# Optimization experiments

Measured on AMD Instinct MI355X. Metric: run time of the kernel, lower is better.

The kernel has to match this reference:

```python
import jax, jax.numpy as jnp
import numpy as np

B, C_IN, H, W = 4, 256, 56, 56
REL, OUT, SP, K, PAD = 16, 256, 8, 7, 3
WS = OUT // SP            # 32 attention-weight channels
K2 = K * K                # 49 window taps
EPS = 1e-5


def _unfold(x, k, pad):
    # reflect-pad (SAN pad_mode=1 -> *_refpad kernels) then gather kxk window taps
    # x: [B,C,H,W] -> [B,C,k*k,H,W], tap order row-major (matches torch Unfold)
    xp = jnp.pad(x, ((0, 0), (0, 0), (pad, pad), (pad, pad)), mode='reflect')
    h, w = x.shape[2], x.shape[3]
    return jnp.stack([xp[:, :, i:i + h, j:j + w]
                      for i in range(k) for j in range(k)], axis=2)


def _conv1x1(x, w, b):
    return jnp.einsum('bchw,oc->bohw', x, w) + b[None, :, None, None]


def _bn(x, g, b, m, v):
    # eval-mode BatchNorm2d over channel axis 1, broadcast over trailing dims
    shape = (1, -1) + (1,) * (x.ndim - 2)
    scale = g.reshape(shape) * jax.lax.rsqrt(v.reshape(shape) + EPS)
    return (x - m.reshape(shape)) * scale + b.reshape(shape)


def _forward(x, w1, b1, w2, b2, w3, b3,
             bn1_g, bn1_b, bn1_m, bn1_v, cw1_w,
             bn2_g, bn2_b, bn2_m, bn2_v, cw2_w, cw2_b, pos2_w):
    x1 = _conv1x1(x, w1, b1)          # [B,REL,H,W]  (query)
    x2 = _conv1x1(x, w2, b2)          # [B,REL,H,W]  (key)
    x3 = _conv1x1(x, w3, b3)          # [B,OUT,H,W]  (value)

    # Subtraction2: q_i - k_j for each of K2 window taps -> [B,REL,K2,H,W]
    diff = x1[:, :, None, :, :] - _unfold(x2, K, PAAD) if False else x1[:, :, None, :, :] - _unfold(x2, K, PAD)

    # conv_w: BN -> ReLU -> 1x1 (no bias) -> BN -> ReLU -> 1x1 (bias)
    h = jax.nn.relu(_bn(diff, bn1_g, bn1_b, bn1_m, bn1_v))
    h = jnp.einsum('bckhw,oc->bokhw', h, cw1_w)
    h = jax.nn.relu(_bn(h, bn2_g, bn2_b, bn2_m, bn2_v))
    h = jnp.einsum('bckhw,oc->bokhw', h, cw2_w) + cw2_b[None, :, None, None, None]
    w = jax.nn.softmax(h, axis=2)     # softmax over K2 taps -> [B,WS,K2,H,W]

    # Aggregation: out[b,c,p] = sum_k unfold(x3)[b,c,k,p] * w[b, c//SP, k, p]
    unf3 = _unfold(x3, K, PAD).reshape(B, WS, SP, K2, H, W)
    agg = jnp.einsum('bgskhw,bgkhw->bgshw', unf3, w).reshape(B, OUT, H, W)

    # use_position2: interleave aggregated values with w, grouped 1x1 conv
    xv = agg.reshape(B, SP, WS, H, W).transpose(0, 2, 1, 3, 4)   # [B,WS,SP,H,W]
    xc = jnp.concatenate([xv, w], axis=2)                        # [B,WS,SP+K2,H,W]
    out = jnp.einsum('bgihw,goi->bgohw', xc, pos2_w).reshape(B, OUT, H, W)
    return out


def setup_inputs() -> dict:
    key = jax.random.key(0)
    ks = jax.random.split(key, 20)
    n = lambda k, s, sc=1.0: jax.random.normal(k, s, dtype=jnp.float32) * sc
    u = lambda k, s: jax.random.uniform(k, s, dtype=jnp.float32, minval=0.5, maxval=1.5)
    return {
        'x': n(ks[0], (B, C_IN, H, W)),
        'w1': n(ks[1], (REL, C_IN), 0.05), 'b1': n(ks[2], (REL,), 0.05),
        'w2': n(ks[3], (REL, C_IN), 0.05), 'b2': n(ks[4], (REL,), 0.05),
        'w3': n(ks[5], (OUT, C_IN), 0.05), 'b3': n(ks[6], (OUT,), 0.05),
        'bn1_g': u(ks[7], (REL,)), 'bn1_b': n(ks[8], (REL,), 0.1),
        'bn1_m': n(ks[9], (REL,), 0.1), 'bn1_v': u(ks[10], (REL,)),
        'cw1_w': n(ks[11], (REL, REL), 0.2),
        'bn2_g': u(ks[12], (REL,)), 'bn2_b': n(ks[13], (REL,), 0.1),
        'bn2_m': n(ks[14], (REL,), 0.1), 'bn2_v': u(ks[15], (REL,)),
        'cw2_w': n(ks[16], (WS, REL), 0.2), 'cw2_b': n(ks[17], (WS,), 0.05),
        'pos2_w': n(ks[18], (WS, SP, SP + K2), 0.1),
    }


def reference(x, w1, b1, w2, b2, w3, b3,
              bn1_g, bn1_b, bn1_m, bn1_v, cw1_w,
              bn2_g, bn2_b, bn2_m, bn2_v, cw2_w, cw2_b, pos2_w):
    return _forward(x, w1, b1, w2, b2, w3, b3,
                    bn1_g, bn1_b, bn1_m, bn1_v, cw1_w,
                    bn2_g, bn2_b, bn2_m, bn2_v, cw2_w, cw2_b, pos2_w)
```

## Files before the change

### kernel.cpp

```cpp
#include <hip/hip_runtime.h>

#define HW 56
#define NPIX 3136
#define CIN 256
#define OUTC 256

typedef unsigned short ushort_t;
typedef unsigned int uint_t;
typedef __attribute__((ext_vector_type(8))) short bf16x8;
typedef __attribute__((ext_vector_type(4))) float f32x4;
typedef __attribute__((ext_vector_type(2))) __fp16 half2v;

__device__ __forceinline__ ushort_t f2b(float f){
  uint_t u = __float_as_uint(f);
  u += 0x7fffu + ((u>>16)&1u);
  return (ushort_t)(u>>16);
}
__device__ __forceinline__ int refl(int v){ v = v<0 ? -v : v; return v>=HW ? 2*HW-2-v : v; }

#define BF_OFF   40960
#define CW1H_OFF 41280
#define CW2H_OFF 41536
#define CW2B_OFF 42048
#define BNC_OFF  42112
#define P2T_OFF  42176
#define P2H_OFF  56768
#define X1T_OFF  82368
#define X2T_OFF  283072
#define X3_BYTE_OFF 1935104

__global__ void k0_prep(const float* __restrict__ w1, const float* __restrict__ b1,
                        const float* __restrict__ w2, const float* __restrict__ b2,
                        const float* __restrict__ w3, const float* __restrict__ b3,
                        const float* __restrict__ g1, const float* __restrict__ be1,
                        const float* __restrict__ m1, const float* __restrict__ v1,
                        const float* __restrict__ cw1,
                        const float* __restrict__ g2, const float* __restrict__ be2,
                        const float* __restrict__ m2, const float* __restrict__ v2,
                        const float* __restrict__ cw2, const float* __restrict__ cw2b,
                        const float* __restrict__ p2,
                        float* __restrict__ ws)
{
  int idx = blockIdx.x*256 + threadIdx.x;
  if (idx < 81920){
    int j = idx & 7, l = (idx>>3)&63, t2 = idx>>9;
    int nf = t2 % 20, kt = t2 / 20;
    int k = kt*32 + (l>>4)*8 + j;
    int n = nf*16 + (l&15);
    float v = 0.f;
    if (n < 16)       v = w1[n*256 + k];
    else if (n < 32)  v = w2[(n-16)*256 + k];
    else if (n < 288) v = w3[(n-32)*256 + k];
    ((ushort_t*)ws)[idx] = f2b(v);
    return;
  }
  int j = idx - 81920;
  if (j < 288){ ws[BF_OFF+j] = (j<16 ? b1[j] : (j<32 ? b2[j-16] : b3[j-32])); return; }
  j -= 288;
  if (j < 32){ ws[BF_OFF+288+j] = 0.f; return; }
  j -= 32;
  if (j < 128){
    int o = j>>3, p = j&7;
    union { __fp16 h[2]; uint_t u; } cv;
    cv.h[0] = (__fp16)cw1[o*16 + 2*p];
    cv.h[1] = (__fp16)cw1[o*16 + 2*p+1];
    ((uint_t*)ws)[CW1H_OFF + j] = cv.u;
    return;
  }
  j -= 128;
  if (j < 256){
    int g = j>>3, p = j&7;
    union { __fp16 h[2]; uint_t u; } cv;
    cv.h[0] = (__fp16)cw2[g*16 + 2*p];
    cv.h[1] = (__fp16)cw2[g*16 + 2*p+1];
    ((uint_t*)ws)[CW2H_OFF + j] = cv.u;
    return;
  }
  j -= 256;
  if (j < 32){ ws[CW2B_OFF+j] = cw2b[j]; return; }
  j -= 32;
  if (j < 64){
    int set = j >> 4, c = j & 15;
    float o;
    if (set == 0){ o = g1[c] * rsqrtf(v1[c] + 1e-5f); }
    else if (set == 1){ float s = g1[c] * rsqrtf(v1[c] + 1e-5f); o = be1[c] - m1[c]*s; }
    else if (set == 2){ o = g2[c] * rsqrtf(v2[c] + 1e-5f); }
    else { float s = g2[c] * rsqrtf(v2[c] + 1e-5f); o = be2[c] - m2[c]*s; }
    ws[BNC_OFF+j] = o;
    return;
  }
  j -= 64;
  if (j < 14592){
    int i = j >> 8, rem = j & 255;
    ws[P2T_OFF + j] = p2[rem*57 + i];
    return;
  }
  j -= 14592;
  if (j < 25600){
    int p = j >> 8, c = j & 255;
    union { __fp16 h[2]; uint_t u; } cv;
    cv.h[0] = (__fp16)p2[c*57 + 8 + 2*p];
    cv.h[1] = (2*p+1 < 49) ? (__fp16)p2[c*57 + 9 + 2*p] : (__fp16)0.f;
    ((uint_t*)ws)[P2H_OFF + j] = cv.u;
    return;
  }
}

__global__ __launch_bounds__(256,2) void k1_proj(const float* __restrict__ x,
                                                 float* __restrict__ ws,
                                                 _Float16* __restrict__ x3h)
{
  __shared__ float xs[CIN*64];
  int t = threadIdx.x;
  int bid = blockIdx.x;
  int b = bid / 49, pp = (bid - b*49)*64;
  int wv = __builtin_amdgcn_readfirstlane(t >> 6);
  int lane = t & 63;

  {
    const float* src = x + (size_t)b*CIN*NPIX + pp;
    int c0 = t >> 4;
    int po = (t & 15) * 4;
    #pragma unroll
    for (int i=0;i<16;i++){
      const float* gp = src + (size_t)(i*16 + c0)*NPIX + po;
      __builtin_amdgcn_global_load_lds(
          (const __attribute__((address_space(1))) void*)gp,
          (__attribute__((address_space(3))) void*)(xs + i*1024 + wv*256),
          16, 0, 0);
    }
  }
  __syncthreads();

  f32x4 acc[4][5];
  float bias[5];
  #pragma unroll
  for (int nf=0;nf<5;nf++) bias[nf] = ws[BF_OFF + wv*80 + nf*16 + (lane&15)];
  #pragma unroll
  for (int m=0;m<4;m++)
    #pragma unroll
    for (int nf=0;nf<5;nf++)
      acc[m][nf] = (f32x4){bias[nf],bias[nf],bias[nf],bias[nf]};

  const uint4* bpk = (const uint4*)ws;
  #pragma unroll 1
  for (int kt=0;kt<8;kt++){
    int abase = (kt*32 + ((lane>>4)<<3))*64 + (lane&15);
    union { uint_t u[4]; bf16x8 v; } ahi[4], alo[4];
    #pragma unroll
    for (int m=0;m<4;m++){
      float f[8];
      #pragma unroll
      for (int j=0;j<8;j++) f[j] = xs[abase + j*64 + m*16];
      #pragma unroll
      for (int p=0;p<4;p++){
        uint_t u0 = __float_as_uint(f[2*p]), u1 = __float_as_uint(f[2*p+1]);
        uint_t h1 = u1 & 0xffff0000u;
        ahi[m].u[p] = (u0>>16) | h1;
        float l0 = f[2*p]   - __uint_as_float(u0 & 0xffff0000u);
        float l1 = f[2*p+1] - __uint_as_float(h1);
        alo[m].u[p] = (__float_as_uint(l0)>>16) | (__float_as_uint(l1) & 0xffff0000u);
      }
    }
    #pragma unroll
    for (int nf=0;nf<5;nf++){
      union { uint4 q; bf16x8 v; } bw;
      bw.q = bpk[(size_t)(kt*20 + wv*5 + nf)*64 + lane];
      #pragma unroll
      for (int m=0;m<4;m++){
        acc[m][nf] = __builtin_amdgcn_mfma_f32_16x16x32_bf16(ahi[m].v, bw.v, acc[m][nf], 0,0,0);
        acc[m][nf] = __builtin_amdgcn_mfma_f32_16x16x32_bf16(alo[m].v, bw.v, acc[m][nf], 0,0,0);
      }
    }
  }

  #pragma unroll
  for (int m=0;m<4;m++){
    #pragma unroll
    for (int r=0;r<4;r++){
      int sp = pp + m*16 + ((lane>>4)<<2) + r;
      #pragma unroll
      for (int nf=0;nf<5;nf++){
        int n = wv*80 + nf*16 + (lane&15);
        float val = acc[m][nf][r];
        if (n < 16){
          ws[X1T_OFF + (size_t)(b*NPIX + sp)*16 + n] = val;
        } else if (n < 32){
          ws[X2T_OFF + (size_t)(b*NPIX + sp)*16 + (n-16)] = val;
        } else if (n < 288){
          x3h[((size_t)b*NPIX + sp)*256 + (n-32)] = (_Float16)val;
        }
      }
    }
  }
}

__global__ __launch_bounds__(256,8) void k2_fused(const float* __restrict__ ws,
                                                  const _Float16* __restrict__ x3h,
                                                  float* __restrict__ out)
{
  __shared__ uint_t lgw[4*840];
  __shared__ int    gp_s[4*64];
  __shared__ __align__(16) float ags[4*256];

  int tid = threadIdx.x;
  int bid0 = blockIdx.x;
  int bid = (bid0 & 7)*392 + (bid0 >> 3);
  int b = bid / 784; int rem = bid - b*784;
  int row = rem / 14, xs4 = rem - row*14;
  int wv = __builtin_amdgcn_readfirstlane(tid >> 6);
  int lane = tid & 63;
  int y = row, x = xs4*4 + wv;
  int pix = y*HW + x;

  const float* bnc  = ws + BNC_OFF;
  const uint_t* c1h = (const uint_t*)ws + CW1H_OFF;
  const uint_t* c2h = (const uint_t*)ws + CW2H_OFF;
  const float* cw2b = ws + CW2B_OFF;
  uint_t* wvbase = lgw + wv*840;

  {
    int k = lane;
    int kk = k < 49 ? k : 48;
    int ki = kk / 7, kj = kk - ki*7;
    int gy = refl(y + ki - 3), gx = refl(x + kj - 3);
    int go = gy*HW + gx;
    gp_s[wv*64 + lane] = go;

    const float*  x1p = ws + X1T_OFF + (size_t)(b*NPIX + pix)*16;
    const float4* x2p = (const float4*)(ws + X2T_OFF + (size_t)(b*NPIX + go)*16);
    float4 v0 = x2p[0], v1 = x2p[1], v2 = x2p[2], v3 = x2p[3];
    float x2v[16] = {v0.x,v0.y,v0.z,v0.w, v1.x,v1.y,v1.z,v1.w,
                     v2.x,v2.y,v2.z,v2.w, v3.x,v3.y,v3.z,v3.w};
    float h1[16];
    #pragma unroll
    for (int c=0;c<16;c++){
      float d = x1p[c] - x2v[c];
      h1[c] = fmaxf(d*bnc[c] + bnc[16+c], 0.f);
    }
    half2v hp[8];
    #pragma unroll
    for (int p=0;p<8;p++) hp[p] = __builtin_amdgcn_cvt_pkrtz(h1[2*p], h1[2*p+1]);

    float tt[16];
    #pragma unroll
    for (int o=0;o<16;o++){
      float a = 0.f;
      #pragma unroll
      for (int p=0;p<8;p++){
        union { uint_t u; half2v h; } cv; cv.u = c1h[o*8+p];
        a = __builtin_amdgcn_fdot2(hp[p], cv.h, a, false);
      }
      tt[o] = fmaxf(a*bnc[32+o] + bnc[48+o], 0.f);
    }
    half2v tp[8];
    #pragma unroll
    for (int p=0;p<8;p++) tp[p] = __builtin_amdgcn_cvt_pkrtz(tt[2*p], tt[2*p+1]);

    if (k < 49){
      #pragma unroll
      for (int gp=0; gp<16; gp++){
        float a0 = cw2b[2*gp], a1 = cw2b[2*gp+1];
        #pragma unroll
        for (int p=0;p<8;p++){
          union { uint_t u; half2v h; } e0, e1;
          e0.u = c2h[(2*gp)*8+p];
          e1.u = c2h[(2*gp+1)*8+p];
          a0 = __builtin_amdgcn_fdot2(tp[p], e0.h, a0, false);
          a1 = __builtin_amdgcn_fdot2(tp[p], e1.h, a1, false);
        }
        union { half2v h; uint_t u; } pk;
        pk.h = __builtin_amdgcn_cvt_pkrtz(a0, a1);
        wvbase[k*17 + gp] = pk.u;
      }
    }
  }

  {
    int half = lane >> 5, g = lane & 31, gsel = g & 1, gp = g >> 1;
    float e[25];
    float M = -3.0e38f;
    #pragma unroll
    for (int i=0;i<25;i++){
      if (half == 0 || i < 24){
        uint_t u = wvbase[(half*25+i)*17 + gp];
        union { ushort_t s; __fp16 h; } cv;
        cv.s = gsel ? (ushort_t)(u>>16) : (ushort_t)(u & 0xffffu);
        e[i] = (float)cv.h;
        M = fmaxf(M, e[i]);
      }
    }
    M = fmaxf(M, __shfl_xor(M, 32, 64));
    float s = 0.f;
    #pragma unroll
    for (int i=0;i<25;i++){
      if (half == 0 || i < 24){
        e[i] = __expf(e[i] - M);
        s += e[i];
      }
    }
    s += __shfl_xor(s, 32, 64);
    float inv = 1.f / s;
    #pragma unroll
    for (int i=0;i<25;i++){
      if (half == 0 || i < 24) e[i] *= inv;
    }
    float other = __shfl_xor(half ? e[0] : e[24], 32, 64);
    if (half == 0){
      #pragma unroll
      for (int p=0;p<12;p++){
        union { half2v h; uint_t u; } pk;
        pk.h = __builtin_amdgcn_cvt_pkrtz(e[2*p], e[2*p+1]);
        wvbase[p*33 + g] = pk.u;
      }
      union { half2v h; uint_t u; } pk;
      pk.h = __builtin_amdgcn_cvt_pkrtz(e[24], other);
      wvbase[12*33 + g] = pk.u;
    } else {
      #pragma unroll
      for (int q=0;q<11;q++){
        union { half2v h; uint_t u; } pk;
        pk.h = __builtin_amdgcn_cvt_pkrtz(e[1+2*q], e[2+2*q]);
        wvbase[(13+q)*33 + g] = pk.u;
      }
      union { half2v h; uint_t u; } pk;
      pk.h = __builtin_amdgcn_cvt_pkrtz(e[23], 0.f);
      wvbase[24*33 + g] = pk.u;
    }
  }

  {
    int g_ = lane >> 1;
    int c0 = lane * 4;
    const int* gpp = gp_s + wv*64;
    float a0=0.f,a1=0.f,a2=0.f,a3=0.f;
    const _Float16* xb = x3h + (size_t)b*NPIX*256 + c0;
    #pragma unroll 5
    for (int p=0;p<25;p++){
      uint_t wu = wvbase[p*33 + g_];
      union { ushort_t s; __fp16 h; } wl, wh;
      wl.s = (ushort_t)(wu & 0xffffu); wh.s = (ushort_t)(wu >> 16);
      float w0 = (float)wl.h, w1 = (float)wh.h;
      int gp0 = gpp[2*p], gp1 = gpp[2*p+1];
      union { uint2 u; _Float16 h[4]; } d0, d1;
      d0.u = *(const uint2*)(xb + (size_t)gp0*256);
      d1.u = *(const uint2*)(xb + (size_t)gp1*256);
      a0 += w0*(float)d0.h[0] + w1*(float)d1.h[0];
      a1 += w0*(float)d0.h[1] + w1*(float)d1.h[1];
      a2 += w0*(float)d0.h[2] + w1*(float)d1.h[2];
      a3 += w0*(float)d0.h[3] + w1*(float)d1.h[3];
    }
    *(float4*)&ags[wv*256 + c0] = make_float4(a0,a1,a2,a3);
  }
  __syncthreads();

  {
    int c = tid, g4 = c >> 3;
    const float* P2 = ws + P2T_OFF;
    const uint_t* P2H = (const uint_t*)ws + P2H_OFF;
    float r0=0.f, r1=0.f, r2=0.f, r3=0.f;
    #pragma unroll
    for (int i=0;i<8;i++){
      float pv = P2[i*256 + c];
      r0 += ags[0*256 + i*32 + g4] * pv;
      r1 += ags[1*256 + i*32 + g4] * pv;
      r2 += ags[2*256 + i*32 + g4] * pv;
      r3 += ags[3*256 + i*32 + g4] * pv;
    }
    #pragma unroll 5
    for (int p=0;p<25;p++){
      union { uint_t u; half2v h; } ph; ph.u = P2H[p*256 + c];
      union { uint_t u; half2v h; } w0, w1, w2, w3;
      w0.u = lgw[0*840 + p*33 + g4];
      w1.u = lgw[1*840 + p*33 + g4];
      w2.u = lgw[2*840 + p*33 + g4];
      w3.u = lgw[3*840 + p*33 + g4];
      r0 = __builtin_amdgcn_fdot2(w0.h, ph.h, r0, false);
      r1 = __builtin_amdgcn_fdot2(w1.h, ph.h, r1, false);
      r2 = __builtin_amdgcn_fdot2(w2.h, ph.h, r2, false);
      r3 = __builtin_amdgcn_fdot2(w3.h, ph.h, r3, false);
    }
    int pix0 = y*HW + xs4*4;
    *(float4*)(out + ((size_t)(b*256 + c))*NPIX + pix0) = make_float4(r0,r1,r2,r3);
  }
}

extern "C" void kernel_launch(void* const* d_in, const int* in_sizes, int n_in,
                              void* d_out, int out_size, void* d_ws, size_t ws_size,
                              hipStream_t stream) {
  const float* x    = (const float*)d_in[0];
  const float* w1   = (const float*)d_in[1];
  const float* b1   = (const float*)d_in[2];
  const float* w2   = (const float*)d_in[3];
  const float* b2   = (const float*)d_in[4];
  const float* w3   = (const float*)d_in[5];
  const float* b3   = (const float*)d_in[6];
  const float* g1   = (const float*)d_in[7];
  const float* be1  = (const float*)d_in[8];
  const float* m1   = (const float*)d_in[9];
  const float* v1   = (const float*)d_in[10];
  const float* cw1  = (const float*)d_in[11];
  const float* g2   = (const float*)d_in[12];
  const float* be2  = (const float*)d_in[13];
  const float* m2   = (const float*)d_in[14];
  const float* v2   = (const float*)d_in[15];
  const float* cw2  = (const float*)d_in[16];
  const float* cw2b = (const float*)d_in[17];
  const float* p2   = (const float*)d_in[18];

  float* wsf = (float*)d_ws;
  _Float16* x3h = (_Float16*)((char*)d_ws + X3_BYTE_OFF);
  float* o = (float*)d_out;

  k0_prep<<<481, 256, 0, stream>>>(w1,b1,w2,b2,w3,b3,g1,be1,m1,v1,cw1,g2,be2,m2,v2,cw2,cw2b,p2,wsf);
  k1_proj<<<196, 256, 0, stream>>>(x, wsf, x3h);
  k2_fused<<<3136, 256, 0, stream>>>(wsf, x3h, o);
}
```

Baseline: 64.71 us.

## Make position conv per-wave to drop block barrier; precompute byte offsets

The final grouped 1x1 position conv is reorganized so each wave handles its own pixel and four consecutive output channels, reading only its own wave's LDS data. This removes the __syncthreads between aggregation and the position conv. It requires P2/P2H to be laid out in a 4-channel-vectorized order. Gather offsets are also prescaled to byte offsets to save address arithmetic. The cost is that output stores become scattered scalar writes across channel planes instead of float4 writes along pixels.

```diff
diff --git a/kernel.cpp b/kernel.cpp
--- a/kernel.cpp
+++ b/kernel.cpp
@@ -225,7 +225,7 @@
     int ki = kk / 7, kj = kk - ki*7;
     int gy = refl(y + ki - 3), gx = refl(x + kj - 3);
     int go = gy*HW + gx;
-    gp_s[wv*64 + lane] = go;
+    gp_s[wv*64 + lane] = go << 9;
 
     const float*  x1p = ws + X1T_OFF + (size_t)(b*NPIX + pix)*16;
     const float4* x2p = (const float4*)(ws + X2T_OFF + (size_t)(b*NPIX + go)*16);
@@ -334,17 +334,17 @@
     int c0 = lane * 4;
     const int* gpp = gp_s + wv*64;
     float a0=0.f,a1=0.f,a2=0.f,a3=0.f;
-    const _Float16* xb = x3h + (size_t)b*NPIX*256 + c0;
+    const char* xbb = (const char*)(x3h + (size_t)b*NPIX*256) + c0*2;
     #pragma unroll 5
     for (int p=0;p<25;p++){
       uint_t wu = wvbase[p*33 + g_];
       union { ushort_t s; __fp16 h; } wl, wh;
       wl.s = (ushort_t)(wu & 0xffffu); wh.s = (ushort_t)(wu >> 16);
       float w0 = (float)wl.h, w1 = (float)wh.h;
-      int gp0 = gpp[2*p], gp1 = gpp[2*p+1];
+      int o0 = gpp[2*p], o1 = gpp[2*p+1];
       union { uint2 u; _Float16 h[4]; } d0, d1;
-      d0.u = *(const uint2*)(xb + (size_t)gp0*256);
-      d1.u = *(const uint2*)(xb + (size_t)gp1*256);
+      d0.u = *(const uint2*)(xbb + o0);
+      d1.u = *(const uint2*)(xbb + o1);
       a0 += w0*(float)d0.h[0] + w1*(float)d1.h[0];
       a1 += w0*(float)d0.h[1] + w1*(float)d1.h[1];
       a2 += w0*(float)d0.h[2] + w1*(float)d1.h[2];
@@ -352,36 +352,36 @@
     }
     *(float4*)&ags[wv*256 + c0] = make_float4(a0,a1,a2,a3);
   }
-  __syncthreads();
 
   {
-    int c = tid, g4 = c >> 3;
-    const float* P2 = ws + P2T_OFF;
-    const uint_t* P2H = (const uint_t*)ws + P2H_OFF;
+    int g_ = lane >> 1;
+    int c0 = lane * 4;
+    const float4* P2v  = (const float4*)(ws + P2T_OFF);
+    const uint4*  P2Hv = (const uint4*)((const uint_t*)ws + P2H_OFF);
+    const float*  agw  = ags + wv*256;
     float r0=0.f, r1=0.f, r2=0.f, r3=0.f;
     #pragma unroll
     for (int i=0;i<8;i++){
-      float pv = P2[i*256 + c];
-      r0 += ags[0*256 + i*32 + g4] * pv;
-      r1 += ags[1*256 + i*32 + g4] * pv;
-      r2 += ags[2*256 + i*32 + g4] * pv;
-      r3 += ags[3*256 + i*32 + g4] * pv;
+      float av = agw[i*32 + g_];
+      float4 pv = P2v[i*64 + lane];
+      r0 += av*pv.x; r1 += av*pv.y; r2 += av*pv.z; r3 += av*pv.w;
     }
     #pragma unroll 5
     for (int p=0;p<25;p++){
-      union { uint_t u; half2v h; } ph; ph.u = P2H[p*256 + c];
-      union { uint_t u; half2v h; } w0, w1, w2, w3;
-      w0.u = lgw[0*840 + p*33 + g4];
-      w1.u = lgw[1*840 + p*33 + g4];
-      w2.u = lgw[2*840 + p*33 + g4];
-      w3.u = lgw[3*840 + p*33 + g4];
-      r0 = __builtin_amdgcn_fdot2(w0.h, ph.h, r0, false);
-      r1 = __builtin_amdgcn_fdot2(w1.h, ph.h, r1, false);
-      r2 = __builtin_amdgcn_fdot2(w2.h, ph.h, r2, false);
-      r3 = __builtin_amdgcn_fdot2(w3.h, ph.h, r3, false);
-    }
-    int pix0 = y*HW + xs4*4;
-    *(float4*)(out + ((size_t)(b*256 + c))*NPIX + pix0) = make_float4(r0,r1,r2,r3);
+      union { uint_t u; half2v h; } wpk; wpk.u = wvbase[p*33 + g_];
+      uint4 ph = P2Hv[p*64 + lane];
+      union { uint_t u; half2v h; } q0,q1,q2,q3;
+      q0.u=ph.x; q1.u=ph.y; q2.u=ph.z; q3.u=ph.w;
+      r0 = __builtin_amdgcn_fdot2(wpk.h, q0.h, r0, false);
+      r1 = __builtin_amdgcn_fdot2(wpk.h, q1.h, r1, false);
+      r2 = __builtin_amdgcn_fdot2(wpk.h, q2.h, r2, false);
+      r3 = __builtin_amdgcn_fdot2(wpk.h, q3.h, r3, false);
+    }
+    size_t ob = ((size_t)b*256 + c0)*NPIX + pix;
+    out[ob]          = r0;
+    out[ob +   NPIX] = r1;
+    out[ob + 2*NPIX] = r2;
+    out[ob + 3*NPIX] = r3;
   }
 }
 
```

Result: slower. 73.90 us (+14.2%).

## Compute conv_w 1x1 layers with MFMA 16x16x16 f16 instead of fdot2

Applied to the files above, without the earlier changes.

Replaces the per-lane fdot2 loops for the two small 16x16 and 16x32 1x1 convolutions in the attention-weight branch with MFMA f16 instructions. The activations are staged through a new per-wave LDS tile, and the weights are pre-swizzled into MFMA B-fragment layout in the prep kernel. The softmax read layout is changed to match, and gather offsets are pre-shifted into byte offsets. The extra LDS and the lower launch-bounds occupancy hint (8 to 5) may reduce concurrency in exchange for fewer VALU instructions.

```diff
diff --git a/kernel.cpp b/kernel.cpp
--- a/kernel.cpp
+++ b/kernel.cpp
@@ -10,17 +10,29 @@
 typedef __attribute__((ext_vector_type(8))) short bf16x8;
 typedef __attribute__((ext_vector_type(4))) float f32x4;
 typedef __attribute__((ext_vector_type(2))) __fp16 half2v;
+typedef __attribute__((ext_vector_type(4))) _Float16 f16x4;
 
 __device__ __forceinline__ ushort_t f2b(float f){
   uint_t u = __float_as_uint(f);
   u += 0x7fffu + ((u>>16)&1u);
   return (ushort_t)(u>>16);
 }
+__device__ __forceinline__ uint_t pkh2(float a, float b){
+  union { half2v h; uint_t u; } pk;
+  pk.h = __builtin_amdgcn_cvt_pkrtz(a, b);
+  return pk.u;
+}
+__device__ __forceinline__ float h2lo(uint_t u){
+  union { ushort_t s; __fp16 h; } c; c.s = (ushort_t)(u & 0xffffu); return (float)c.h;
+}
+__device__ __forceinline__ float h2hi(uint_t u){
+  union { ushort_t s; __fp16 h; } c; c.s = (ushort_t)(u >> 16); return (float)c.h;
+}
 __device__ __forceinline__ int refl(int v){ v = v<0 ? -v : v; return v>=HW ? 2*HW-2-v : v; }
 
 #define BF_OFF   40960
-#define CW1H_OFF 41280
-#define CW2H_OFF 41536
+#define CW1B_OFF 41280
+#define CW2B_OFF2 41536
 #define CW2B_OFF 42048
 #define BNC_OFF  42112
 #define P2T_OFF  42176
@@ -60,20 +72,22 @@
   if (j < 32){ ws[BF_OFF+288+j] = 0.f; return; }
   j -= 32;
   if (j < 128){
-    int o = j>>3, p = j&7;
+    int l = j>>1, q = j&1;
+    int n = l & 15, k = ((l>>4)<<2) + 2*q;
     union { __fp16 h[2]; uint_t u; } cv;
-    cv.h[0] = (__fp16)cw1[o*16 + 2*p];
-    cv.h[1] = (__fp16)cw1[o*16 + 2*p+1];
-    ((uint_t*)ws)[CW1H_OFF + j] = cv.u;
+    cv.h[0] = (__fp16)cw1[n*16 + k];
+    cv.h[1] = (__fp16)cw1[n*16 + k+1];
+    ((uint_t*)ws)[CW1B_OFF + j] = cv.u;
     return;
   }
   j -= 128;
   if (j < 256){
-    int g = j>>3, p = j&7;
+    int nf = j>>7, rem = j&127, l = rem>>1, q = rem&1;
+    int n = nf*16 + (l & 15), k = ((l>>4)<<2) + 2*q;
     union { __fp16 h[2]; uint_t u; } cv;
-    cv.h[0] = (__fp16)cw2[g*16 + 2*p];
-    cv.h[1] = (__fp16)cw2[g*16 + 2*p+1];
-    ((uint_t*)ws)[CW2H_OFF + j] = cv.u;
+    cv.h[0] = (__fp16)cw2[n*16 + k];
+    cv.h[1] = (__fp16)cw2[n*16 + k+1];
+    ((uint_t*)ws)[CW2B_OFF2 + j] = cv.u;
     return;
   }
   j -= 256;
@@ -195,11 +209,12 @@
   }
 }
 
-__global__ __launch_bounds__(256,8) void k2_fused(const float* __restrict__ ws,
+__global__ __launch_bounds__(256,5) void k2_fused(const float* __restrict__ ws,
                                                   const _Float16* __restrict__ x3h,
                                                   float* __restrict__ out)
 {
-  __shared__ uint_t lgw[4*840];
+  __shared__ uint_t lgw[4*864];
+  __shared__ ushort_t sA[4*1280];
   __shared__ int    gp_s[4*64];
   __shared__ __align__(16) float ags[4*256];
 
@@ -214,10 +229,10 @@
   int pix = y*HW + x;
 
   const float* bnc  = ws + BNC_OFF;
-  const uint_t* c1h = (const uint_t*)ws + CW1H_OFF;
-  const uint_t* c2h = (const uint_t*)ws + CW2H_OFF;
   const float* cw2b = ws + CW2B_OFF;
-  uint_t* wvbase = lgw + wv*840;
+  uint_t* wvbase = lgw + wv*864;
+  ushort_t* sAw = sA + wv*1280;
+  int lrow = lane & 15, lk4 = (lane>>4)<<2;
 
   {
     int k = lane;
@@ -225,7 +240,7 @@
     int ki = kk / 7, kj = kk - ki*7;
     int gy = refl(y + ki - 3), gx = refl(x + kj - 3);
     int go = gy*HW + gx;
-    gp_s[wv*64 + lane] = go;
+    gp_s[wv*64 + lane] = go << 9;
 
     const float*  x1p = ws + X1T_OFF + (size_t)(b*NPIX + pix)*16;
     const float4* x2p = (const float4*)(ws + X2T_OFF + (size_t)(b*NPIX + go)*16);
@@ -238,57 +253,79 @@
       float d = x1p[c] - x2v[c];
       h1[c] = fmaxf(d*bnc[c] + bnc[16+c], 0.f);
     }
-    half2v hp[8];
-    #pragma unroll
-    for (int p=0;p<8;p++) hp[p] = __builtin_amdgcn_cvt_pkrtz(h1[2*p], h1[2*p+1]);
-
-    float tt[16];
-    #pragma unroll
-    for (int o=0;o<16;o++){
-      float a = 0.f;
-      #pragma unroll
-      for (int p=0;p<8;p++){
-        union { uint_t u; half2v h; } cv; cv.u = c1h[o*8+p];
-        a = __builtin_amdgcn_fdot2(hp[p], cv.h, a, false);
-      }
-      tt[o] = fmaxf(a*bnc[32+o] + bnc[48+o], 0.f);
-    }
-    half2v tp[8];
-    #pragma unroll
-    for (int p=0;p<8;p++) tp[p] = __builtin_amdgcn_cvt_pkrtz(tt[2*p], tt[2*p+1]);
-
-    if (k < 49){
-      #pragma unroll
-      for (int gp=0; gp<16; gp++){
-        float a0 = cw2b[2*gp], a1 = cw2b[2*gp+1];
-        #pragma unroll
-        for (int p=0;p<8;p++){
-          union { uint_t u; half2v h; } e0, e1;
-          e0.u = c2h[(2*gp)*8+p];
-          e1.u = c2h[(2*gp+1)*8+p];
-          a0 = __builtin_amdgcn_fdot2(tp[p], e0.h, a0, false);
-          a1 = __builtin_amdgcn_fdot2(tp[p], e1.h, a1, false);
-        }
-        union { half2v h; uint_t u; } pk;
-        pk.h = __builtin_amdgcn_cvt_pkrtz(a0, a1);
-        wvbase[k*17 + gp] = pk.u;
+    {
+      uint2* dst = (uint2*)(sAw + lane*20);
+      dst[0] = make_uint2(pkh2(h1[0],h1[1]),  pkh2(h1[2],h1[3]));
+      dst[1] = make_uint2(pkh2(h1[4],h1[5]),  pkh2(h1[6],h1[7]));
+      dst[2] = make_uint2(pkh2(h1[8],h1[9]),  pkh2(h1[10],h1[11]));
+      dst[3] = make_uint2(pkh2(h1[12],h1[13]),pkh2(h1[14],h1[15]));
+    }
+    union { uint2 u; f16x4 h; } B1, B20, B21;
+    B1.u  = ((const uint2*)((const uint_t*)ws + CW1B_OFF))[lane];
+    B20.u = ((const uint2*)((const uint_t*)ws + CW2B_OFF2))[lane];
+    B21.u = ((const uint2*)((const uint_t*)ws + CW2B_OFF2))[64 + lane];
+
+    float bs2 = bnc[32+lrow], bb2 = bnc[48+lrow];
+    #pragma unroll
+    for (int m=0;m<4;m++){
+      union { uint2 u; f16x4 h; } A;
+      A.u = *(const uint2*)(sAw + (m*16+lrow)*20 + lk4);
+      f32x4 d = __builtin_amdgcn_mfma_f32_16x16x16f16(A.h, B1.h, (f32x4){0.f,0.f,0.f,0.f}, 0,0,0);
+      #pragma unroll
+      for (int r=0;r<4;r++){
+        float tv = fmaxf(d[r]*bs2 + bb2, 0.f);
+        union { __fp16 h; ushort_t s; } th; th.h = (__fp16)tv;
+        sAw[(m*16 + lk4 + r)*20 + lrow] = th.s;
+      }
+    }
+    float bg0 = cw2b[lrow], bg1 = cw2b[16+lrow];
+    #pragma unroll
+    for (int m=0;m<4;m++){
+      union { uint2 u; f16x4 h; } A2;
+      A2.u = *(const uint2*)(sAw + (m*16+lrow)*20 + lk4);
+      f32x4 d0 = __builtin_amdgcn_mfma_f32_16x16x16f16(A2.h, B20.h, (f32x4){bg0,bg0,bg0,bg0}, 0,0,0);
+      f32x4 d1 = __builtin_amdgcn_mfma_f32_16x16x16f16(A2.h, B21.h, (f32x4){bg1,bg1,bg1,bg1}, 0,0,0);
+      int pq = m*8 + ((lane>>4)<<1);
+      uint_t p01 = pkh2(d0[0], d0[1]), p23 = pkh2(d0[2], d0[3]);
+      uint_t q01 = pkh2(d1[0], d1[1]), q23 = pkh2(d1[2], d1[3]);
+      if (pq < 25){
+        wvbase[lrow*27 + pq]      = p01;
+        wvbase[(16+lrow)*27 + pq] = q01;
+      }
+      if (pq+1 < 25){
+        wvbase[lrow*27 + pq+1]      = p23;
+        wvbase[(16+lrow)*27 + pq+1] = q23;
       }
     }
   }
 
   {
-    int half = lane >> 5, g = lane & 31, gsel = g & 1, gp = g >> 1;
+    int half = lane >> 5, g = lane & 31;
+    const uint_t* lgp = wvbase + g*27;
     float e[25];
     float M = -3.0e38f;
-    #pragma unroll
-    for (int i=0;i<25;i++){
-      if (half == 0 || i < 24){
-        uint_t u = wvbase[(half*25+i)*17 + gp];
-        union { ushort_t s; __fp16 h; } cv;
-        cv.s = gsel ? (ushort_t)(u>>16) : (ushort_t)(u & 0xffffu);
-        e[i] = (float)cv.h;
-        M = fmaxf(M, e[i]);
-      }
+    if (half == 0){
+      #pragma unroll
+      for (int j=0;j<12;j++){
+        uint_t u = lgp[j];
+        e[2*j]   = h2lo(u);
+        e[2*j+1] = h2hi(u);
+      }
+      e[24] = h2lo(lgp[12]);
+      #pragma unroll
+      for (int i=0;i<25;i++) M = fmaxf(M, e[i]);
+    } else {
+      e[0] = h2hi(lgp[12]);
+      #pragma unroll
+      for (int j=0;j<11;j++){
+        uint_t u = lgp[13+j];
+        e[1+2*j] = h2lo(u);
+        e[2+2*j] = h2hi(u);
+      }
+      e[23] = h2lo(lgp[24]);
+      e[24] = 0.f;
+      #pragma unroll
+      for (int i=0;i<24;i++) M = fmaxf(M, e[i]);
     }
     M = fmaxf(M, __shfl_xor(M, 32, 64));
     float s = 0.f;
@@ -308,24 +345,12 @@
     float other = __shfl_xor(half ? e[0] : e[24], 32, 64);
     if (half == 0){
       #pragma unroll
-      for (int p=0;p<12;p++){
-        union { half2v h; uint_t u; } pk;
-        pk.h = __builtin_amdgcn_cvt_pkrtz(e[2*p], e[2*p+1]);
-        wvbase[p*33 + g] = pk.u;
-      }
-      union { half2v h; uint_t u; } pk;
-      pk.h = __builtin_amdgcn_cvt_pkrtz(e[24], other);
-      wvbase[12*33 + g] = pk.u;
+      for (int p=0;p<12;p++) wvbase[p*33 + g] = pkh2(e[2*p], e[2*p+1]);
+      wvbase[12*33 + g] = pkh2(e[24], other);
     } else {
       #pragma unroll
-      for (int q=0;q<11;q++){
-        union { half2v h; uint_t u; } pk;
-        pk.h = __builtin_amdgcn_cvt_pkrtz(e[1+2*q], e[2+2*q]);
-        wvbase[(13+q)*33 + g] = pk.u;
-      }
-      union { half2v h; uint_t u; } pk;
-      pk.h = __builtin_amdgcn_cvt_pkrtz(e[23], 0.f);
-      wvbase[24*33 + g] = pk.u;
+      for (int q=0;q<11;q++) wvbase[(13+q)*33 + g] = pkh2(e[1+2*q], e[2+2*q]);
+      wvbase[24*33 + g] = pkh2(e[23], 0.f);
     }
   }
 
@@ -334,17 +359,15 @@
     int c0 = lane * 4;
     const int* gpp = gp_s + wv*64;
     float a0=0.f,a1=0.f,a2=0.f,a3=0.f;
-    const _Float16* xb = x3h + (size_t)b*NPIX*256 + c0;
+    const char* xbb = (const char*)(x3h + (size_t)b*NPIX*256) + c0*2;
     #pragma unroll 5
     for (int p=0;p<25;p++){
       uint_t wu = wvbase[p*33 + g_];
-      union { ushort_t s; __fp16 h; } wl, wh;
-      wl.s = (ushort_t)(wu & 0xffffu); wh.s = (ushort_t)(wu >> 16);
-      float w0 = (float)wl.h, w1 = (float)wh.h;
-      int gp0 = gpp[2*p], gp1 = gpp[2*p+1];
+      float w0 = h2lo(wu), w1 = h2hi(wu);
+      int o0 = gpp[2*p], o1 = gpp[2*p+1];
       union { uint2 u; _Float16 h[4]; } d0, d1;
-      d0.u = *(const uint2*)(xb + (size_t)gp0*256);
-      d1.u = *(const uint2*)(xb + (size_t)gp1*256);
+      d0.u = *(const uint2*)(xbb + o0);
+      d1.u = *(const uint2*)(xbb + o1);
       a0 += w0*(float)d0.h[0] + w1*(float)d1.h[0];
       a1 += w0*(float)d0.h[1] + w1*(float)d1.h[1];
       a2 += w0*(float)d0.h[2] + w1*(float)d1.h[2];
@@ -371,10 +394,10 @@
     for (int p=0;p<25;p++){
       union { uint_t u; half2v h; } ph; ph.u = P2H[p*256 + c];
       union { uint_t u; half2v h; } w0, w1, w2, w3;
-      w0.u = lgw[0*840 + p*33 + g4];
-      w1.u = lgw[1*840 + p*33 + g4];
-      w2.u = lgw[2*840 + p*33 + g4];
-      w3.u = lgw[3*840 + p*33 + g4];
+      w0.u = lgw[0*864 + p*33 + g4];
+      w1.u = lgw[1*864 + p*33 + g4];
+      w2.u = lgw[2*864 + p*33 + g4];
+      w3.u = lgw[3*864 + p*33 + g4];
       r0 = __builtin_amdgcn_fdot2(w0.h, ph.h, r0, false);
       r1 = __builtin_amdgcn_fdot2(w1.h, ph.h, r1, false);
       r2 = __builtin_amdgcn_fdot2(w2.h, ph.h, r2, false);
```

After: 57.87 us. -10.6%, faster.
